# Optimization experiments

Hardware: AMD Instinct MI355X
Metric: run time of the kernel (lower is better)

Reference implementation:

```python
import jax, jax.numpy as jnp
import numpy as np

GROUPS = 6  # attn_group in Stack

def setup_inputs() -> dict:
    key = jax.random.key(0)
    k0, k1, k2, k3, k4 = jax.random.split(key, 5)
    B, S, IN, OUT, K = 2, 2048, 512, 768, 31
    fan = (2.0 / IN) ** 0.5  # kaiming_normal fan_out-ish scale
    x = jax.random.normal(k0, (B, S, IN), jnp.float32)
    W_q = jax.random.normal(k1, (OUT, IN), jnp.float32) * fan
    W_k = jax.random.normal(k2, (OUT, IN), jnp.float32) * fan
    W_v = jax.random.normal(k3, (OUT, IN), jnp.float32) * fan
    rel = jax.random.normal(k4, (OUT, K), jnp.float32)
    return {"x": x, "W_q": W_q, "W_k": W_k, "W_v": W_v, "rel": rel}

def reference(x, W_q, W_k, W_v, rel):
    B, S, _ = x.shape
    OUT, K = rel.shape
    pad = (K - 1) // 2
    d = OUT // GROUPS
    # projections
    q = x @ W_q.T                                   # [B,S,OUT]
    xp = jnp.pad(x, ((0, 0), (pad, pad), (0, 0)))    # pad seq dim
    k = xp @ W_k.T                                  # [B,S+K-1,OUT]
    v = xp @ W_v.T
    # unfold: window of size K per query position (stride 1)
    idx = jnp.arange(S)[:, None] + jnp.arange(K)[None, :]   # [S,K]
    k_win = k[:, idx, :] + rel.T                    # [B,S,K,OUT], rel bias (out,K)->(K,out)
    v_win = v[:, idx, :]                            # [B,S,K,OUT]
    k_win = k_win.reshape(B, S, K, GROUPS, d)
    v_win = v_win.reshape(B, S, K, GROUPS, d)
    qg = q.reshape(B, S, GROUPS, d)
    energy = jnp.einsum('bsgd,bskgd->bsgk', qg, k_win)       # QK dot over head dim
    attn = jax.nn.softmax(energy, axis=-1)                   # softmax over window
    out = jnp.einsum('bsgk,bskgd->bsgd', attn, v_win).reshape(B, S, OUT)
    return out, attn  # attn matches torch attention.squeeze(3): [B,S,groups,K]
```

## Files before the change

kernel.cpp:

```cpp
#include <hip/hip_runtime.h>
#include <hip/hip_bf16.h>

#define S_LEN 2048
#define B_SZ 2
#define IN_DIM 512
#define OUT_DIM 768
#define KWIN 31
#define PAD 15
#define NGROUP 6
#define DHEAD 128
#define M_TOT 4096
#define N_TOT 2304
#define QK_W 1536

typedef __attribute__((ext_vector_type(8))) __bf16 bf16x8;
typedef __attribute__((ext_vector_type(8))) unsigned short u16x8;
typedef __attribute__((ext_vector_type(4))) float f32x4;

static __device__ __forceinline__ unsigned short f2bf(float f) {
  unsigned int u = __float_as_uint(f);
  unsigned int r = (u + 0x7fffu + ((u >> 16) & 1u)) >> 16;
  return (unsigned short)r;
}
static __device__ __forceinline__ float bf2f(unsigned short h) {
  return __uint_as_float(((unsigned int)h) << 16);
}

__global__ __launch_bounds__(256) void prep_kernel(
    const float* __restrict__ x,
    const float* __restrict__ Wq, const float* __restrict__ Wk, const float* __restrict__ Wv,
    const float* __restrict__ rel,
    unsigned short* __restrict__ xhi, unsigned short* __restrict__ xlo,
    unsigned short* __restrict__ whi, unsigned short* __restrict__ wlo,
    unsigned short* __restrict__ relThi, unsigned short* __restrict__ relTlo,
    unsigned short* __restrict__ zpage) {
  const int bid = blockIdx.x;
  const int tid = threadIdx.x;
  if (bid < 2048) {
    int i = bid * 256 + tid;
    float4 v = ((const float4*)x)[i];
    unsigned short h0 = f2bf(v.x), h1 = f2bf(v.y), h2 = f2bf(v.z), h3 = f2bf(v.w);
    ((ushort4*)xhi)[i] = make_ushort4(h0, h1, h2, h3);
    ((ushort4*)xlo)[i] = make_ushort4(f2bf(v.x - bf2f(h0)), f2bf(v.y - bf2f(h1)),
                                      f2bf(v.z - bf2f(h2)), f2bf(v.w - bf2f(h3)));
  } else if (bid < 3200) {
    int i = (bid - 2048) * 256 + tid;
    int e = i * 4;
    const int per = OUT_DIM * IN_DIM;
    const float* src = (e < per) ? Wq : (e < 2 * per) ? Wk : Wv;
    int rem = (e < per) ? e : (e < 2 * per) ? e - per : e - 2 * per;
    float4 v = *(const float4*)(src + rem);
    unsigned short h0 = f2bf(v.x), h1 = f2bf(v.y), h2 = f2bf(v.z), h3 = f2bf(v.w);
    ((ushort4*)whi)[i] = make_ushort4(h0, h1, h2, h3);
    ((ushort4*)wlo)[i] = make_ushort4(f2bf(v.x - bf2f(h0)), f2bf(v.y - bf2f(h1)),
                                      f2bf(v.z - bf2f(h2)), f2bf(v.w - bf2f(h3)));
  } else if (bid < 3293) {
    int idx = (bid - 3200) * 256 + tid;
    int kk = idx / OUT_DIM;
    int o = idx - kk * OUT_DIM;
    float v = rel[o * KWIN + kk];
    unsigned short h = f2bf(v);
    relThi[idx] = h;
    relTlo[idx] = f2bf(v - bf2f(h));
  } else {
    if (tid < 128) zpage[tid] = 0;
  }
}

#define SLOTB 49152

static __device__ __forceinline__ int swz32(int O) {
  return O ^ (((O >> 7) & 3) << 4);
}

#define MFMA16(AF, BF) \
  _Pragma("unroll") for (int mi = 0; mi < 4; ++mi) \
  _Pragma("unroll") for (int ni = 0; ni < 4; ++ni) \
    acc[mi][ni] = __builtin_amdgcn_mfma_f32_16x16x32_bf16( \
        AF[mi], BF[ni], acc[mi][ni], 0, 0, 0);

#define READ_AHI() _Pragma("unroll") for (int mi = 0; mi < 4; ++mi) ahi[mi] = *(const bf16x8*)(slot + aoff[mi]);
#define READ_ALO() _Pragma("unroll") for (int mi = 0; mi < 4; ++mi) alo[mi] = *(const bf16x8*)(slot + 16384 + aoff[mi]);
#define READ_WHI() _Pragma("unroll") for (int ni = 0; ni < 4; ++ni) whi[ni] = *(const bf16x8*)(slot + 32768 + boff[ni]);
#define READ_WLO() _Pragma("unroll") for (int ni = 0; ni < 4; ++ni) wlo[ni] = *(const bf16x8*)(slot + 40960 + boff[ni]);

#define END_BARRIER() \
  __builtin_amdgcn_s_barrier(); \
  asm volatile("" ::: "memory");

__global__ __launch_bounds__(512, 2) void gemm_kernel(
    const unsigned short* __restrict__ Ahi, const unsigned short* __restrict__ Alo,
    const unsigned short* __restrict__ Whi, const unsigned short* __restrict__ Wlo,
    unsigned short* __restrict__ qkhi, unsigned short* __restrict__ qklo,
    unsigned short* __restrict__ vTw) {
  __shared__ unsigned short lds_u16[73728];
  char* ldsb = (char*)lds_u16;
  const int tid = threadIdx.x;
  const int wid = tid >> 6, lane = tid & 63;
  const int elr = lane & 15, elq = lane >> 4;
  const int wm = wid >> 1, wn = wid & 1;

  int aoff[4], boff[4];
#pragma unroll
  for (int mi = 0; mi < 4; ++mi)
    aoff[mi] = swz32((wm * 64 + mi * 16 + elr) * 64 + elq * 16);
#pragma unroll
  for (int ni = 0; ni < 4; ++ni)
    boff[ni] = swz32((wn * 64 + ni * 16 + elr) * 64 + elq * 16);

  const int strow = tid >> 2;
  const int stcol = (((tid & 3) ^ ((tid >> 3) & 3)) << 3);

  auto stage8k = [&](char* slot, int RO, int j, const unsigned short* src,
                     int grow0, int kloc) {
    const unsigned short* g = src + (size_t)(grow0 + j * 128 + strow) * IN_DIM + kloc + stcol;
    __builtin_amdgcn_global_load_lds((const __attribute__((address_space(1))) void*)g,
        (__attribute__((address_space(3))) void*)(slot + RO + j * 8192 + wid * 1024), 16, 0, 0);
  };

  f32x4 acc[4][4] = {};
  bf16x8 ahi[4], whi[4], alo[4], wlo[4];

  const int bid = blockIdx.x;

  if (bid < 192) {
    const int bm = bid & 15, ct = bid >> 4;
    const int row0 = bm << 8, col0 = ct << 7;

    auto stageChunk = [&](int cc) {
      char* s = ldsb + (cc % 3) * SLOTB;
      const int pk = cc << 5;
      stage8k(s, 0, 0, Ahi, row0, pk);      stage8k(s, 0, 1, Ahi, row0, pk);
      stage8k(s, 16384, 0, Alo, row0, pk);  stage8k(s, 16384, 1, Alo, row0, pk);
      stage8k(s, 32768, 0, Whi, col0, pk);  stage8k(s, 40960, 0, Wlo, col0, pk);
    };

    stageChunk(0);
    stageChunk(1);
    asm volatile("s_waitcnt vmcnt(6)" ::: "memory");
    END_BARRIER()

    for (int c = 0; c < 16; ++c) {
      char* slot = ldsb + (c % 3) * SLOTB;
      READ_AHI()
      READ_WHI()
      READ_ALO()
      READ_WLO()
      const bool pref = (c + 2) < 16;
      if (pref) stageChunk(c + 2);
      __builtin_amdgcn_s_setprio(1);
      MFMA16(ahi, whi)
      MFMA16(alo, whi)
      MFMA16(ahi, wlo)
      __builtin_amdgcn_s_setprio(0);
      if (pref) { asm volatile("s_waitcnt vmcnt(6)" ::: "memory"); }
      else      { asm volatile("s_waitcnt vmcnt(0)" ::: "memory"); }
      END_BARRIER()
    }

    const int elg = elq * 4;
#pragma unroll
    for (int mi = 0; mi < 4; ++mi)
#pragma unroll
      for (int ni = 0; ni < 4; ++ni) {
        int ncol = col0 + wn * 64 + ni * 16 + elr;
        size_t rbase = (size_t)(row0 + wm * 64 + mi * 16 + elg);
#pragma unroll
        for (int j = 0; j < 4; ++j) {
          float v = acc[mi][ni][j];
          unsigned short h = f2bf(v);
          size_t idx = (rbase + j) * QK_W + ncol;
          qkhi[idx] = h;
          qklo[idx] = f2bf(v - bf2f(h));
        }
      }
  } else {
    const int bid2 = bid - 192;
    const int bm = bid2 & 15, grp = bid2 >> 4;
    const int row0 = bm << 8;
    auto vcol = [&](int ci) { return 1536 + ((grp * 2 + (ci >> 4)) << 7); };

    auto stageChunkV = [&](int cc) {
      char* s = ldsb + (cc % 3) * SLOTB;
      const int pk = (cc & 15) << 5;
      stage8k(s, 0, 0, Ahi, row0, pk);  stage8k(s, 0, 1, Ahi, row0, pk);
      stage8k(s, 32768, 0, Whi, vcol(cc), pk);
    };

    stageChunkV(0);
    stageChunkV(1);
    asm volatile("s_waitcnt vmcnt(3)" ::: "memory");
    END_BARRIER()

    for (int ci = 0; ci < 32; ++ci) {
      char* slot = ldsb + (ci % 3) * SLOTB;
      READ_AHI()
      READ_WHI()
      const bool pref = (ci + 2) < 32;
      if (pref) stageChunkV(ci + 2);
      __builtin_amdgcn_s_setprio(1);
      MFMA16(ahi, whi)
      __builtin_amdgcn_s_setprio(0);
      if (pref) { asm volatile("s_waitcnt vmcnt(3)" ::: "memory"); }
      else      { asm volatile("s_waitcnt vmcnt(0)" ::: "memory"); }
      END_BARRIER()

      if ((ci & 15) == 15) {
        const int col0 = vcol(ci);
        const int elg = elq * 4;
#pragma unroll
        for (int mi = 0; mi < 4; ++mi)
#pragma unroll
          for (int ni = 0; ni < 4; ++ni) {
            int d = col0 - 1536 + wn * 64 + ni * 16 + elr;
            int srw = row0 + wm * 64 + mi * 16 + elg;
            ushort4 pk4;
            pk4.x = f2bf(acc[mi][ni][0]); pk4.y = f2bf(acc[mi][ni][1]);
            pk4.z = f2bf(acc[mi][ni][2]); pk4.w = f2bf(acc[mi][ni][3]);
            *(ushort4*)(vTw + (size_t)d * M_TOT + srw) = pk4;
            acc[mi][ni] = (f32x4){0.f, 0.f, 0.f, 0.f};
          }
      }
    }
  }
}

__global__ __launch_bounds__(256, 2) void attn_kernel(
    const unsigned short* __restrict__ qkhi, const unsigned short* __restrict__ qklo,
    const unsigned short* __restrict__ vT,
    const unsigned short* __restrict__ relThi, const unsigned short* __restrict__ relTlo,
    const unsigned short* __restrict__ zpage,
    float* __restrict__ out, float* __restrict__ attn_out) {
  __shared__ __attribute__((aligned(16))) unsigned short smem[40960];
  char* smb = (char*)smem;
  float* Elds = (float*)(smb + 69632);

  const int tid = threadIdx.x;
  const int wid = tid >> 6, lane = tid & 63;
  const int bid = (blockIdx.x & 7) * 96 + (blockIdx.x >> 3);
  const int tile = bid & 63;
  const int g = (bid >> 6) % NGROUP;
  const int b = bid / (64 * NGROUP);
  const int s0 = tile * 32;
  const size_t rowbase = (size_t)b * S_LEN;
  const int elr = lane & 15, elq = lane >> 4;

  {
    const int wrow = wid * 4 + (lane >> 4);
    const int kcb = lane & 15;
#pragma unroll
    for (int arr = 0; arr < 2; ++arr) {
      const unsigned short* src = arr ? qklo : qkhi;
      const unsigned short* rsrc = arr ? relTlo : relThi;
      const int ldsbase = arr ? 24576 : 0;
#pragma unroll
      for (int i = 0; i < 6; ++i) {
        int w = i * 16 + wrow;
        int scb = (kcb ^ (w & 7)) * 8;
        const unsigned short* gp;
        if (w < 62) {
          int r = s0 - 15 + w;
          gp = (r >= 0 && r < S_LEN)
             ? src + (size_t)(rowbase + r) * QK_W + OUT_DIM + g * DHEAD + scb
             : zpage + scb;
        } else if (w < 93) {
          gp = rsrc + (w - 62) * OUT_DIM + g * DHEAD + scb;
        } else {
          gp = zpage + scb;
        }
        __builtin_amdgcn_global_load_lds((const __attribute__((address_space(1))) void*)gp,
            (__attribute__((address_space(3))) void*)(smb + ldsbase + (i * 16 + wid * 4) * 256 + (lane & 15) * 16 + (lane >> 4) * 256),
            16, 0, 0);
      }
    }
  }
  {
    const unsigned short* vsrc = vT + (size_t)g * DHEAD * M_TOT + (size_t)b * S_LEN;
    const int drow = wid * 8 + (lane >> 3);
    const int vcb = lane & 7;
#pragma unroll
    for (int i = 0; i < 4; ++i) {
      int d = i * 32 + drow;
      int sl = s0 - 16 + (vcb ^ (d & 7)) * 8;
      const unsigned short* gp = (sl >= 0 && sl < S_LEN)
        ? vsrc + (size_t)d * M_TOT + sl
        : zpage + (vcb ^ (d & 7)) * 8;
      __builtin_amdgcn_global_load_lds((const __attribute__((address_space(1))) void*)gp,
          (__attribute__((address_space(3))) void*)(smb + 49152 + (i * 32 + wid * 8) * 128 + (lane >> 3) * 128 + (lane & 7) * 16),
          16, 0, 0);
    }
  }
  {
    int O = tid * 16;
    O ^= (O >> 3) & 0x70;
    u16x8 z = {};
    *(u16x8*)(smb + 65536 + O) = z;
  }

  const int rf = wid & 1;
  const int cb3 = 3 * (wid >> 1);
  bf16x8 qh[4], ql[4];
  {
    size_t qrow = rowbase + s0 + rf * 16 + elr;
    const unsigned short* qb  = qkhi + qrow * QK_W + g * DHEAD + elq * 8;
    const unsigned short* qb2 = qklo + qrow * QK_W + g * DHEAD + elq * 8;
#pragma unroll
    for (int ks = 0; ks < 4; ++ks) {
      qh[ks] = *(const bf16x8*)(qb + ks * 32);
      ql[ks] = *(const bf16x8*)(qb2 + ks * 32);
    }
  }
  __syncthreads();

#pragma unroll
  for (int cf = 0; cf < 3; ++cf) {
    int c = cb3 + cf;
    f32x4 ea = {};
#pragma unroll
    for (int ks = 0; ks < 4; ++ks) {
      int O = (c * 16 + elr) * 256 + ks * 64 + elq * 16;
      int Os = O ^ ((O >> 4) & 0x70);
      bf16x8 kh = *(const bf16x8*)(smb + Os);
      bf16x8 kl = *(const bf16x8*)(smb + 24576 + Os);
      __builtin_amdgcn_s_setprio(1);
      ea = __builtin_amdgcn_mfma_f32_16x16x32_bf16(qh[ks], kh, ea, 0, 0, 0);
      ea = __builtin_amdgcn_mfma_f32_16x16x32_bf16(ql[ks], kh, ea, 0, 0, 0);
      ea = __builtin_amdgcn_mfma_f32_16x16x32_bf16(qh[ks], kl, ea, 0, 0, 0);
      __builtin_amdgcn_s_setprio(0);
    }
#pragma unroll
    for (int j = 0; j < 4; ++j)
      Elds[(rf * 16 + elq * 4 + j) * 96 + c * 16 + elr] = ea[j];
  }
  __syncthreads();

  {
    const int kkl = lane & 31;
    const int half = lane >> 5;
    const int kkc = (kkl < 31) ? kkl : 30;
#pragma unroll
    for (int p = 0; p < 4; ++p) {
      int si = p * 8 + wid * 2 + half;
      float e = Elds[si * 96 + si + kkc] + Elds[si * 96 + 62 + kkc];
      if (kkl == 31) e = -INFINITY;
      float m = e;
#pragma unroll
      for (int off = 16; off > 0; off >>= 1) m = fmaxf(m, __shfl_xor(m, off, 32));
      float pr = __expf(e - m);
      float sum = pr;
#pragma unroll
      for (int off = 16; off > 0; off >>= 1) sum += __shfl_xor(sum, off, 32);
      float a = pr / sum;
      if (kkl < 31) {
        attn_out[((rowbase + s0 + si) * NGROUP + g) * KWIN + kkl] = a;
        int O = si * 128 + (si + kkl + 1) * 2;
        O ^= (O >> 3) & 0x70;
        *(unsigned short*)(smb + 65536 + O) = f2bf(a);
      }
    }
  }
  __syncthreads();

  {
    const int pcb = 4 * (wid >> 1);
    f32x4 pa[4] = {};
#pragma unroll
    for (int ks = 0; ks < 2; ++ks) {
      int AO = (rf * 16 + elr) * 128 + ks * 64 + elq * 16;
      AO ^= (AO >> 3) & 0x70;
      bf16x8 afr = *(const bf16x8*)(smb + 65536 + AO);
      __builtin_amdgcn_s_setprio(1);
#pragma unroll
      for (int cf = 0; cf < 4; ++cf) {
        int VO = ((pcb + cf) * 16 + elr) * 128 + ks * 64 + elq * 16;
        VO ^= (VO >> 3) & 0x70;
        bf16x8 vfr = *(const bf16x8*)(smb + 49152 + VO);
        pa[cf] = __builtin_amdgcn_mfma_f32_16x16x32_bf16(afr, vfr, pa[cf], 0, 0, 0);
      }
      __builtin_amdgcn_s_setprio(0);
    }
#pragma unroll
    for (int cf = 0; cf < 4; ++cf)
#pragma unroll
      for (int j = 0; j < 4; ++j)
        out[(rowbase + s0 + rf * 16 + elq * 4 + j) * OUT_DIM + g * DHEAD + pcb * 16 + cf * 16 + elr]
            = pa[cf][j];
  }
}

extern "C" void kernel_launch(void* const* d_in, const int* in_sizes, int n_in,
                              void* d_out, int out_size, void* d_ws, size_t ws_size,
                              hipStream_t stream) {
  const float* x   = (const float*)d_in[0];
  const float* Wq  = (const float*)d_in[1];
  const float* Wk  = (const float*)d_in[2];
  const float* Wv  = (const float*)d_in[3];
  const float* rel = (const float*)d_in[4];

  char* ws = (char*)d_ws;
  unsigned short* Ahi    = (unsigned short*)(ws);
  unsigned short* Alo    = (unsigned short*)(ws + 4194304);
  unsigned short* Whi    = (unsigned short*)(ws + 8388608);
  unsigned short* Wlo    = (unsigned short*)(ws + 10747904);
  unsigned short* relThi = (unsigned short*)(ws + 13107200);
  unsigned short* relTlo = (unsigned short*)(ws + 13154816);
  unsigned short* qkhi   = (unsigned short*)(ws + 13202432);
  unsigned short* qklo   = (unsigned short*)(ws + 25785344);
  unsigned short* vTw    = (unsigned short*)(ws + 38368256);
  unsigned short* zpage  = (unsigned short*)(ws + 44659712);

  float* outp = (float*)d_out;
  float* attn = outp + (size_t)B_SZ * S_LEN * OUT_DIM;

  prep_kernel<<<3294, 256, 0, stream>>>(x, Wq, Wk, Wv, rel, Ahi, Alo, Whi, Wlo,
                                        relThi, relTlo, zpage);
  gemm_kernel<<<240, 512, 0, stream>>>(Ahi, Alo, Whi, Wlo, qkhi, qklo, vTw);
  attn_kernel<<<768, 256, 0, stream>>>(qkhi, qklo, vTw, relThi, relTlo, zpage, outp, attn);
}
```

Baseline: 54.36 us.

## Load GEMM weight fragments directly from global into registers, double-buffered

The projection GEMM no longer stages the weight tile (hi/lo bf16 split) through LDS. Each wave now loads its own W fragments from global memory straight into registers, one chunk ahead, using ping-pong register buffers. Only the activation tiles still go through the 3-slot LDS ring, which shrinks LDS use and may allow higher occupancy. The cost is uncoalesced per-lane 16-byte global loads, duplicated W reads across the waves that share a column slice, and more register pressure.

New measurement: 79.04 us. 45.4% more time.

```diff
diff --git a/kernel.cpp b/kernel.cpp
--- a/kernel.cpp
+++ b/kernel.cpp
@@ -67,7 +67,7 @@
   }
 }
 
-#define SLOTB 49152
+#define SLOTB 32768
 
 static __device__ __forceinline__ int swz32(int O) {
   return O ^ (((O >> 7) & 3) << 4);
@@ -81,8 +81,6 @@
 
 #define READ_AHI() _Pragma("unroll") for (int mi = 0; mi < 4; ++mi) ahi[mi] = *(const bf16x8*)(slot + aoff[mi]);
 #define READ_ALO() _Pragma("unroll") for (int mi = 0; mi < 4; ++mi) alo[mi] = *(const bf16x8*)(slot + 16384 + aoff[mi]);
-#define READ_WHI() _Pragma("unroll") for (int ni = 0; ni < 4; ++ni) whi[ni] = *(const bf16x8*)(slot + 32768 + boff[ni]);
-#define READ_WLO() _Pragma("unroll") for (int ni = 0; ni < 4; ++ni) wlo[ni] = *(const bf16x8*)(slot + 40960 + boff[ni]);
 
 #define END_BARRIER() \
   __builtin_amdgcn_s_barrier(); \
@@ -93,20 +91,17 @@
     const unsigned short* __restrict__ Whi, const unsigned short* __restrict__ Wlo,
     unsigned short* __restrict__ qkhi, unsigned short* __restrict__ qklo,
     unsigned short* __restrict__ vTw) {
-  __shared__ unsigned short lds_u16[73728];
+  __shared__ unsigned short lds_u16[49152];
   char* ldsb = (char*)lds_u16;
   const int tid = threadIdx.x;
   const int wid = tid >> 6, lane = tid & 63;
   const int elr = lane & 15, elq = lane >> 4;
   const int wm = wid >> 1, wn = wid & 1;
 
-  int aoff[4], boff[4];
+  int aoff[4];
 #pragma unroll
   for (int mi = 0; mi < 4; ++mi)
     aoff[mi] = swz32((wm * 64 + mi * 16 + elr) * 64 + elq * 16);
-#pragma unroll
-  for (int ni = 0; ni < 4; ++ni)
-    boff[ni] = swz32((wn * 64 + ni * 16 + elr) * 64 + elq * 16);
 
   const int strow = tid >> 2;
   const int stcol = (((tid & 3) ^ ((tid >> 3) & 3)) << 3);
@@ -119,43 +114,59 @@
   };
 
   f32x4 acc[4][4] = {};
-  bf16x8 ahi[4], whi[4], alo[4], wlo[4];
+  bf16x8 ahi[4], alo[4];
+  bf16x8 whA[4], wlA[4], whB[4], wlB[4];
 
   const int bid = blockIdx.x;
 
   if (bid < 192) {
     const int bm = bid & 15, ct = bid >> 4;
     const int row0 = bm << 8, col0 = ct << 7;
-
-    auto stageChunk = [&](int cc) {
+    const size_t wrow = (size_t)(col0 + wn * 64) * IN_DIM;
+
+    auto loadW = [&](int cc, bf16x8 (&th)[4], bf16x8 (&tl)[4]) {
+      const int pk = cc << 5;
+#pragma unroll
+      for (int ni = 0; ni < 4; ++ni) {
+        size_t off = wrow + (size_t)(ni * 16 + elr) * IN_DIM + pk + elq * 8;
+        th[ni] = *(const bf16x8*)(Whi + off);
+        tl[ni] = *(const bf16x8*)(Wlo + off);
+      }
+    };
+
+    auto stageChunkA = [&](int cc) {
       char* s = ldsb + (cc % 3) * SLOTB;
       const int pk = cc << 5;
       stage8k(s, 0, 0, Ahi, row0, pk);      stage8k(s, 0, 1, Ahi, row0, pk);
       stage8k(s, 16384, 0, Alo, row0, pk);  stage8k(s, 16384, 1, Alo, row0, pk);
-      stage8k(s, 32768, 0, Whi, col0, pk);  stage8k(s, 40960, 0, Wlo, col0, pk);
-    };
-
-    stageChunk(0);
-    stageChunk(1);
-    asm volatile("s_waitcnt vmcnt(6)" ::: "memory");
-    END_BARRIER()
-
-    for (int c = 0; c < 16; ++c) {
+    };
+
+    auto chunkBody = [&](int c, bf16x8 (&curh)[4], bf16x8 (&curl)[4],
+                         bf16x8 (&nxth)[4], bf16x8 (&nxtl)[4]) {
       char* slot = ldsb + (c % 3) * SLOTB;
       READ_AHI()
-      READ_WHI()
       READ_ALO()
-      READ_WLO()
-      const bool pref = (c + 2) < 16;
-      if (pref) stageChunk(c + 2);
+      if (c + 1 < 16) loadW(c + 1, nxth, nxtl);
+      if (c + 2 < 16) stageChunkA(c + 2);
       __builtin_amdgcn_s_setprio(1);
-      MFMA16(ahi, whi)
-      MFMA16(alo, whi)
-      MFMA16(ahi, wlo)
+      MFMA16(ahi, curh)
+      MFMA16(alo, curh)
+      MFMA16(ahi, curl)
       __builtin_amdgcn_s_setprio(0);
-      if (pref) { asm volatile("s_waitcnt vmcnt(6)" ::: "memory"); }
-      else      { asm volatile("s_waitcnt vmcnt(0)" ::: "memory"); }
+      if (c + 2 < 16)      { asm volatile("s_waitcnt vmcnt(12)" ::: "memory"); }
+      else if (c + 1 < 16) { asm volatile("s_waitcnt vmcnt(8)" ::: "memory"); }
       END_BARRIER()
+    };
+
+    loadW(0, whA, wlA);
+    stageChunkA(0);
+    stageChunkA(1);
+    asm volatile("s_waitcnt vmcnt(4)" ::: "memory");
+    END_BARRIER()
+
+    for (int c = 0; c < 16; c += 2) {
+      chunkBody(c, whA, wlA, whB, wlB);
+      chunkBody(c + 1, whB, wlB, whA, wlA);
     }
 
     const int elg = elq * 4;
@@ -180,47 +191,60 @@
     const int row0 = bm << 8;
     auto vcol = [&](int ci) { return 1536 + ((grp * 2 + (ci >> 4)) << 7); };
 
+    auto loadWv = [&](int cc, bf16x8 (&th)[4]) {
+      const int pk = (cc & 15) << 5;
+      const size_t wrow = (size_t)(vcol(cc) + wn * 64) * IN_DIM;
+#pragma unroll
+      for (int ni = 0; ni < 4; ++ni)
+        th[ni] = *(const bf16x8*)(Whi + wrow + (size_t)(ni * 16 + elr) * IN_DIM + pk + elq * 8);
+    };
+
     auto stageChunkV = [&](int cc) {
       char* s = ldsb + (cc % 3) * SLOTB;
       const int pk = (cc & 15) << 5;
       stage8k(s, 0, 0, Ahi, row0, pk);  stage8k(s, 0, 1, Ahi, row0, pk);
-      stage8k(s, 32768, 0, Whi, vcol(cc), pk);
-    };
-
+    };
+
+    auto epiV = [&](int ci) {
+      const int col0 = vcol(ci);
+      const int elg = elq * 4;
+#pragma unroll
+      for (int mi = 0; mi < 4; ++mi)
+#pragma unroll
+        for (int ni = 0; ni < 4; ++ni) {
+          int d = col0 - 1536 + wn * 64 + ni * 16 + elr;
+          int srw = row0 + wm * 64 + mi * 16 + elg;
+          ushort4 pk4;
+          pk4.x = f2bf(acc[mi][ni][0]); pk4.y = f2bf(acc[mi][ni][1]);
+          pk4.z = f2bf(acc[mi][ni][2]); pk4.w = f2bf(acc[mi][ni][3]);
+          *(ushort4*)(vTw + (size_t)d * M_TOT + srw) = pk4;
+          acc[mi][ni] = (f32x4){0.f, 0.f, 0.f, 0.f};
+        }
+    };
+
+    auto chunkBodyV = [&](int ci, bf16x8 (&cur)[4], bf16x8 (&nxt)[4]) {
+      char* slot = ldsb + (ci % 3) * SLOTB;
+      READ_AHI()
+      if (ci + 1 < 32) loadWv(ci + 1, nxt);
+      if (ci + 2 < 32) stageChunkV(ci + 2);
+      __builtin_amdgcn_s_setprio(1);
+      MFMA16(ahi, cur)
+      __builtin_amdgcn_s_setprio(0);
+      if (ci + 2 < 32)      { asm volatile("s_waitcnt vmcnt(6)" ::: "memory"); }
+      else if (ci + 1 < 32) { asm volatile("s_waitcnt vmcnt(4)" ::: "memory"); }
+      END_BARRIER()
+      if ((ci & 15) == 15) epiV(ci);
+    };
+
+    loadWv(0, whA);
     stageChunkV(0);
     stageChunkV(1);
-    asm volatile("s_waitcnt vmcnt(3)" ::: "memory");
+    asm volatile("s_waitcnt vmcnt(2)" ::: "memory");
     END_BARRIER()
 
-    for (int ci = 0; ci < 32; ++ci) {
-      char* slot = ldsb + (ci % 3) * SLOTB;
-      READ_AHI()
-      READ_WHI()
-      const bool pref = (ci + 2) < 32;
-      if (pref) stageChunkV(ci + 2);
-      __builtin_amdgcn_s_setprio(1);
-      MFMA16(ahi, whi)
-      __builtin_amdgcn_s_setprio(0);
-      if (pref) { asm volatile("s_waitcnt vmcnt(3)" ::: "memory"); }
-      else      { asm volatile("s_waitcnt vmcnt(0)" ::: "memory"); }
-      END_BARRIER()
-
-      if ((ci & 15) == 15) {
-        const int col0 = vcol(ci);
-        const int elg = elq * 4;
-#pragma unroll
-        for (int mi = 0; mi < 4; ++mi)
-#pragma unroll
-          for (int ni = 0; ni < 4; ++ni) {
-            int d = col0 - 1536 + wn * 64 + ni * 16 + elr;
-            int srw = row0 + wm * 64 + mi * 16 + elg;
-            ushort4 pk4;
-            pk4.x = f2bf(acc[mi][ni][0]); pk4.y = f2bf(acc[mi][ni][1]);
-            pk4.z = f2bf(acc[mi][ni][2]); pk4.w = f2bf(acc[mi][ni][3]);
-            *(ushort4*)(vTw + (size_t)d * M_TOT + srw) = pk4;
-            acc[mi][ni] = (f32x4){0.f, 0.f, 0.f, 0.f};
-          }
-      }
+    for (int ci = 0; ci < 32; ci += 2) {
+      chunkBodyV(ci, whA, whB);
+      chunkBodyV(ci + 1, whB, whA);
     }
   }
 }
```
